# Kernel optimization log

Hardware: AMD Instinct MI355X
Metric: run time of the kernel (lower is better)

## Reference

```python
import jax, jax.numpy as jnp
import numpy as np

D = 256      # d_model
H = 8        # n_heads
L = 6        # n_layers
F = 1024     # ffn_hidden
MAXB = 50    # max_boids
S = MAXB + 3 # seq len: CLS + ctx + predator + boids
B = 4096
VH = 256     # value_hidden_dim
DH = D // H


def setup_inputs() -> dict:
    key = jax.random.key(0)
    ks = jax.random.split(key, 20)
    r = lambda i, shape: jax.random.normal(ks[i], shape, jnp.float32) * 0.02
    return {
        "observation": jax.random.normal(ks[0], (B, 4 + 4 * MAXB), jnp.float32),
        "cls_emb": r(1, (D,)), "type_cls": r(2, (D,)), "type_ctx": r(3, (D,)),
        "type_pred": r(4, (D,)), "type_boid": r(5, (D,)),
        "ctx_W": r(6, (2, D)), "ctx_b": jnp.zeros((D,), jnp.float32),
        "pred_W": r(7, (4, D)), "pred_b": jnp.zeros((D,), jnp.float32),
        "boid_W": r(8, (4, D)), "boid_b": jnp.zeros((D,), jnp.float32),
        "qkv_W": r(9, (L, D, 3 * D)), "qkv_b": jnp.zeros((L, 3 * D), jnp.float32),
        "out_W": r(10, (L, D, D)), "out_b": jnp.zeros((L, D), jnp.float32),
        "ln1_g": jnp.ones((L, D), jnp.float32), "ln1_b": jnp.zeros((L, D), jnp.float32),
        "ffn_W1": r(11, (L, D, F)), "ffn_b1": jnp.zeros((L, F), jnp.float32),
        "ffn_W2": r(12, (L, F, D)), "ffn_b2": jnp.zeros((L, D), jnp.float32),
        "ln2_g": jnp.ones((L, D), jnp.float32), "ln2_b": jnp.zeros((L, D), jnp.float32),
        "proj_W": r(13, (D, 2)), "proj_b": jnp.zeros((2,), jnp.float32),
        "vh_W1": r(14, (D, VH)), "vh_b1": jnp.zeros((VH,), jnp.float32),
        "vh_W2": r(15, (VH, VH)), "vh_b2": jnp.zeros((VH,), jnp.float32),
        "vh_W3": r(16, (VH, 1)), "vh_b3": jnp.zeros((1,), jnp.float32),
    }


def _ln(x, g, b):
    m = jnp.mean(x, axis=-1, keepdims=True)
    v = jnp.mean((x - m) ** 2, axis=-1, keepdims=True)
    return (x - m) * jax.lax.rsqrt(v + 1e-5) * g + b


def reference(observation, cls_emb, type_cls, type_ctx, type_pred, type_boid,
              ctx_W, ctx_b, pred_W, pred_b, boid_W, boid_b,
              qkv_W, qkv_b, out_W, out_b, ln1_g, ln1_b,
              ffn_W1, ffn_b1, ffn_W2, ffn_b2, ln2_g, ln2_b,
              proj_W, proj_b, vh_W1, vh_b1, vh_W2, vh_b2, vh_W3, vh_b3):
    Bn = observation.shape[0]
    ctx = observation[:, :2]                                   # [B,2]
    pred = jnp.concatenate([observation[:, 2:4],
                            jnp.zeros_like(observation[:, :2])], axis=-1)  # [B,4]
    boids = observation[:, 4:].reshape(Bn, MAXB, 4)            # [B,MAXB,4]

    # All-zero boid slots are skipped; valid boids are packed to the front
    # (stable order preserved), then zero-padded -- vectorized via stable argsort.
    valid = jnp.any(boids != 0, axis=-1)                       # [B,MAXB]
    order = jnp.argsort(~valid, axis=1, stable=True)           # valid first
    packed = jnp.take_along_axis(boids, order[:, :, None], axis=1)
    vs = jnp.take_along_axis(valid, order, axis=1)             # [B,MAXB]

    cls_tok = jnp.broadcast_to(cls_emb + type_cls, (Bn, 1, D))
    ctx_tok = (ctx @ ctx_W + ctx_b + type_ctx)[:, None, :]
    pred_tok = (pred @ pred_W + pred_b + type_pred)[:, None, :]
    boid_tok = (packed @ boid_W + boid_b + type_boid) * vs[:, :, None]  # pad -> zeros
    x = jnp.concatenate([cls_tok, ctx_tok, pred_tok, boid_tok], axis=1)  # [B,S,D]

    pad = jnp.concatenate([jnp.zeros((Bn, 3), bool), ~vs], axis=1)       # [B,S]
    neg = jnp.where(pad, -1e9, 0.0)[:, None, None, :]                    # [B,1,1,S]

    scale = 1.0 / np.sqrt(DH)
    for i in range(L):  # post-LN encoder layers (ReLU FFN)
        qkv = x @ qkv_W[i] + qkv_b[i]                                    # [B,S,3D]
        q, k, v = jnp.split(qkv, 3, axis=-1)
        q = q.reshape(Bn, S, H, DH).transpose(0, 2, 1, 3)
        k = k.reshape(Bn, S, H, DH).transpose(0, 2, 1, 3)
        v = v.reshape(Bn, S, H, DH).transpose(0, 2, 1, 3)
        scores = jnp.einsum('bhqd,bhkd->bhqk', q, k) * scale + neg
        a = jax.nn.softmax(scores, axis=-1)
        o = jnp.einsum('bhqk,bhkd->bhqd', a, v).transpose(0, 2, 1, 3).reshape(Bn, S, D)
        x = _ln(x + o @ out_W[i] + out_b[i], ln1_g[i], ln1_b[i])
        h = jax.nn.relu(x @ ffn_W1[i] + ffn_b1[i])
        x = _ln(x + h @ ffn_W2[i] + ffn_b2[i], ln2_g[i], ln2_b[i])

    cls_f = x[:, 0]                                                      # [B,D]
    action_mean = jnp.tanh(cls_f @ proj_W + proj_b)                      # [B,2]
    h = jax.nn.relu(cls_f @ vh_W1 + vh_b1)
    h = jax.nn.relu(h @ vh_W2 + vh_b2)
    value = h @ vh_W3 + vh_b3                                            # [B,1]
    return jnp.concatenate([action_mean, value], axis=-1)                # [B,3]
```

## Files before the change

### kernel.cpp

```cpp
#include <hip/hip_runtime.h>
#include <hip/hip_bf16.h>
#include <stdint.h>

typedef unsigned short u16;
typedef short s16x8 __attribute__((ext_vector_type(8)));
typedef float f32x4 __attribute__((ext_vector_type(4)));

#define D_ 256
#define H_ 8
#define L_ 6
#define F_ 1024
#define MAXB_ 50
#define S_ 53
#define B_ 4096

__device__ __forceinline__ u16 f2b(float f){
  __hip_bfloat16 h = __float2bfloat16(f);
  return *reinterpret_cast<u16*>(&h);
}
__device__ __forceinline__ float b2f(u16 u){
  __hip_bfloat16 h = *reinterpret_cast<__hip_bfloat16*>(&u);
  return __bfloat162float(h);
}

__device__ __forceinline__ void gload16(const void* g, void* l){
  __builtin_amdgcn_global_load_lds((__attribute__((address_space(1))) void*)(g),
                                   (__attribute__((address_space(3))) void*)(l), 16, 0, 0);
}

__global__ __launch_bounds__(256) void prep_weights(
    const float* __restrict__ qkvW, const float* __restrict__ outW,
    const float* __restrict__ w1,   const float* __restrict__ w2,
    u16* __restrict__ qkvT, u16* __restrict__ outT,
    u16* __restrict__ w1T,  u16* __restrict__ w2T)
{
  const int i = blockIdx.x * 256 + threadIdx.x;
  if (i < L_*768*256) {
    const int l = i / (768*256); const int r = i % (768*256);
    const int n = r >> 8; const int k = r & 255;
    qkvT[i] = f2b(qkvW[((size_t)l*256 + k)*768 + n]);
  }
  if (i < L_*256*256) {
    const int l = i >> 16; const int r = i & 65535;
    const int n = r >> 8; const int k = r & 255;
    outT[i] = f2b(outW[((size_t)l*256 + k)*256 + n]);
  }
  if (i < L_*1024*256) {
    const int l = i / (1024*256); const int r = i % (1024*256);
    const int n = r >> 8; const int k = r & 255;
    w1T[i] = f2b(w1[((size_t)l*256 + k)*1024 + n]);
  }
  if (i < L_*256*1024) {
    const int l = i / (256*1024); const int r = i % (256*1024);
    const int n = r >> 10; const int k = r & 1023;
    w2T[i] = f2b(w2[((size_t)l*1024 + k)*256 + n]);
  }
}

__global__ __launch_bounds__(256) void embed_kernel(
    const float* __restrict__ obs,
    const float* __restrict__ cls_emb, const float* __restrict__ type_cls,
    const float* __restrict__ type_ctx, const float* __restrict__ type_pred,
    const float* __restrict__ type_boid,
    const float* __restrict__ ctxW, const float* __restrict__ ctxb,
    const float* __restrict__ predW, const float* __restrict__ predb,
    const float* __restrict__ boidW, const float* __restrict__ boidb,
    u16* __restrict__ xbf, int* __restrict__ nvalid)
{
  const int b = blockIdx.x, tid = threadIdx.x;
  __shared__ float obs_s[204];
  __shared__ int perm_s[MAXB_];
  __shared__ int count_s;
  const float* orow = obs + (size_t)b * 204;
  if (tid < 204) obs_s[tid] = orow[tid];
  __syncthreads();
  if (tid < 64) {
    const int j = tid;
    bool flag = false;
    if (j < MAXB_) {
      const float a0=obs_s[4+4*j], a1=obs_s[5+4*j], a2=obs_s[6+4*j], a3=obs_s[7+4*j];
      flag = (a0!=0.f)||(a1!=0.f)||(a2!=0.f)||(a3!=0.f);
    }
    const unsigned long long m = __ballot(flag);
    if (flag) perm_s[__popcll(m & ((1ull<<j)-1ull))] = j;
    if (j == 0) { count_s = __popcll(m); nvalid[b] = __popcll(m); }
  }
  __syncthreads();
  const int cnt = count_s;
  const int d = tid;
  for (int s = 0; s < S_; ++s) {
    float v;
    if (s == 0)      v = cls_emb[d] + type_cls[d];
    else if (s == 1) v = obs_s[0]*ctxW[d] + obs_s[1]*ctxW[256+d] + ctxb[d] + type_ctx[d];
    else if (s == 2) v = obs_s[2]*predW[d] + obs_s[3]*predW[256+d] + predb[d] + type_pred[d];
    else {
      const int j = s - 3;
      if (j < cnt) {
        const int bj = perm_s[j];
        v = obs_s[4+4*bj]*boidW[d] + obs_s[5+4*bj]*boidW[256+d]
          + obs_s[6+4*bj]*boidW[512+d] + obs_s[7+4*bj]*boidW[768+d]
          + boidb[d] + type_boid[d];
      } else v = 0.f;
    }
    xbf[((size_t)b*S_ + s)*256 + d] = f2b(v);
  }
}

template<bool RELU>
__global__ __launch_bounds__(256, 2) void gemm_bias_kernel(
    const u16* __restrict__ A, const u16* __restrict__ Bt,
    const float* __restrict__ bias, u16* __restrict__ C,
    int N, int K)
{
  __shared__ __attribute__((aligned(16))) u16 As[2][128*64];
  __shared__ __attribute__((aligned(16))) u16 Bs[2][128*64];
  const int tid = threadIdx.x;
  const int w = tid >> 6, lane = tid & 63;
  const int wr = w >> 1, wc = w & 1;
  const int lm = lane & 15, lg = lane >> 4;
  const int lrow = lane >> 3;
  const int lxor = ((lane & 7) ^ lrow) * 8;
  const int m0 = blockIdx.x * 128, n0 = blockIdx.y * 128;
  const int cb0 = (lg*16) ^ ((lm & 7) << 4);
  const int cb1 = (64 + lg*16) ^ ((lm & 7) << 4);

  f32x4 acc[4][4];
  #pragma unroll
  for (int m=0;m<4;m++)
    #pragma unroll
    for (int n=0;n<4;n++)
      #pragma unroll
      for (int t=0;t<4;t++) acc[m][n][t] = 0.f;

  #pragma unroll
  for (int j=0;j<4;j++){
    const int chunk = w*4 + j;
    const int row = chunk*8 + lrow;
    gload16(A  + (size_t)(m0+row)*K + lxor, &As[0][chunk*512]);
    gload16(Bt + (size_t)(n0+row)*K + lxor, &Bs[0][chunk*512]);
  }
  __syncthreads();

  const int NT = K >> 6;
  for (int t = 0; t < NT; ++t) {
    const int cur = t & 1;
    if (t + 1 < NT) {
      const int k0 = (t+1) << 6;
      #pragma unroll
      for (int j=0;j<4;j++){
        const int chunk = w*4 + j;
        const int row = chunk*8 + lrow;
        gload16(A  + (size_t)(m0+row)*K + k0 + lxor, &As[cur^1][chunk*512]);
        gload16(Bt + (size_t)(n0+row)*K + k0 + lxor, &Bs[cur^1][chunk*512]);
      }
    }
    const char* Ab = (const char*)As[cur];
    const char* Bb = (const char*)Bs[cur];
    #pragma unroll
    for (int kk=0;kk<2;kk++){
      const int cb = kk ? cb1 : cb0;
      s16x8 af[4], bfr[4];
      #pragma unroll
      for (int m=0;m<4;m++) af[m]  = *reinterpret_cast<const s16x8*>(Ab + (wr*64 + m*16 + lm)*128 + cb);
      #pragma unroll
      for (int n=0;n<4;n++) bfr[n] = *reinterpret_cast<const s16x8*>(Bb + (wc*64 + n*16 + lm)*128 + cb);
      #pragma unroll
      for (int m=0;m<4;m++)
        #pragma unroll
        for (int n=0;n<4;n++)
          acc[m][n] = __builtin_amdgcn_mfma_f32_16x16x32_bf16(af[m], bfr[n], acc[m][n], 0, 0, 0);
    }
    __syncthreads();
  }

  #pragma unroll
  for (int n=0;n<4;n++){
    const int col = n0 + wc*64 + n*16 + lm;
    const float bv = bias[col];
    #pragma unroll
    for (int m=0;m<4;m++){
      const int r0 = m0 + wr*64 + m*16 + lg*4;
      #pragma unroll
      for (int j=0;j<4;j++){
        float v = acc[m][n][j] + bv;
        if (RELU) v = fmaxf(v, 0.f);
        C[(size_t)(r0+j)*N + col] = f2b(v);
      }
    }
  }
}

__global__ __launch_bounds__(64) void attn_kernel(
    const u16* __restrict__ qkv, u16* __restrict__ O, const int* __restrict__ nvalid)
{
  const int bh = blockIdx.x;
  const int b = bh >> 3, h = bh & 7;
  const int lane = threadIdx.x;
  const int lm = lane & 15, lg = lane >> 4;
  __shared__ __attribute__((aligned(16))) u16 Pl[64*72];
  __shared__ __attribute__((aligned(16))) u16 VT[32*72];
  const size_t base = (size_t)b * S_ * 768;

  s16x8 aQ[4], aK[4];
  #pragma unroll
  for (int t=0;t<4;t++){
    const int r = t*16 + lm;
    if (r < S_){
      aQ[t] = *reinterpret_cast<const s16x8*>(&qkv[base + (size_t)r*768 +       h*32 + lg*8]);
      aK[t] = *reinterpret_cast<const s16x8*>(&qkv[base + (size_t)r*768 + 256 + h*32 + lg*8]);
    } else {
      #pragma unroll
      for (int i=0;i<8;i++){ aQ[t][i]=0; aK[t][i]=0; }
    }
  }
  {
    const int s = lane;
    #pragma unroll
    for (int i4=0;i4<4;i4++){
      s16x8 v;
      if (s < S_) v = *reinterpret_cast<const s16x8*>(&qkv[base + (size_t)s*768 + 512 + h*32 + i4*8]);
      else {
        #pragma unroll
        for (int i=0;i<8;i++) v[i]=0;
      }
      #pragma unroll
      for (int t=0;t<8;t++) VT[(i4*8+t)*72 + s] = (u16)v[t];
    }
  }
  f32x4 zf;
  #pragma unroll
  for (int t=0;t<4;t++) zf[t] = 0.f;
  f32x4 sc[4][4];
  #pragma unroll
  for (int qi=0;qi<4;qi++)
    #pragma unroll
    for (int kj=0;kj<4;kj++)
      sc[qi][kj] = __builtin_amdgcn_mfma_f32_16x16x32_bf16(aQ[qi], aK[kj], zf, 0, 0, 0);

  const int T = 3 + nvalid[b];
  const float scale = 0.17677669529663689f;
  __syncthreads();

  #pragma unroll
  for (int qi=0;qi<4;qi++){
    #pragma unroll
    for (int j=0;j<4;j++){
      float v[4];
      #pragma unroll
      for (int kj=0;kj<4;kj++)
        v[kj] = sc[qi][kj][j]*scale + ((kj*16+lm) < T ? 0.f : -1e9f);
      float mx = fmaxf(fmaxf(v[0],v[1]), fmaxf(v[2],v[3]));
      mx = fmaxf(mx, __shfl_xor(mx, 1));
      mx = fmaxf(mx, __shfl_xor(mx, 2));
      mx = fmaxf(mx, __shfl_xor(mx, 4));
      mx = fmaxf(mx, __shfl_xor(mx, 8));
      float e[4]; float sum = 0.f;
      #pragma unroll
      for (int kj=0;kj<4;kj++){ e[kj] = __expf(v[kj]-mx); sum += e[kj]; }
      sum += __shfl_xor(sum, 1);
      sum += __shfl_xor(sum, 2);
      sum += __shfl_xor(sum, 4);
      sum += __shfl_xor(sum, 8);
      const float inv = 1.f / sum;
      const int q = qi*16 + lg*4 + j;
      #pragma unroll
      for (int kj=0;kj<4;kj++) Pl[q*72 + kj*16 + lm] = f2b(e[kj]*inv);
    }
  }
  __syncthreads();

  s16x8 bV[2][2];
  #pragma unroll
  for (int c=0;c<2;c++)
    #pragma unroll
    for (int dj=0;dj<2;dj++)
      bV[c][dj] = *reinterpret_cast<const s16x8*>(&VT[(dj*16+lm)*72 + c*32 + lg*8]);

  f32x4 oa[4][2];
  #pragma unroll
  for (int qi=0;qi<4;qi++)
    #pragma unroll
    for (int dj=0;dj<2;dj++)
      #pragma unroll
      for (int t=0;t<4;t++) oa[qi][dj][t] = 0.f;

  #pragma unroll
  for (int qi=0;qi<4;qi++){
    #pragma unroll
    for (int c=0;c<2;c++){
      const s16x8 aP = *reinterpret_cast<const s16x8*>(&Pl[(qi*16+lm)*72 + c*32 + lg*8]);
      #pragma unroll
      for (int dj=0;dj<2;dj++)
        oa[qi][dj] = __builtin_amdgcn_mfma_f32_16x16x32_bf16(aP, bV[c][dj], oa[qi][dj], 0, 0, 0);
    }
  }
  #pragma unroll
  for (int qi=0;qi<4;qi++)
    #pragma unroll
    for (int dj=0;dj<2;dj++)
      #pragma unroll
      for (int j=0;j<4;j++){
        const int q = qi*16 + lg*4 + j;
        if (q < S_)
          O[((size_t)(b*S_ + q))*256 + h*32 + dj*16 + lm] = f2b(oa[qi][dj][j]);
      }
}

__global__ __launch_bounds__(512, 2) void gemm_ln_kernel(
    const u16* __restrict__ A, const u16* __restrict__ Bt,
    const float* __restrict__ bias, const float* __restrict__ lng, const float* __restrict__ lnb,
    u16* __restrict__ xbf, int K)
{
  __shared__ __attribute__((aligned(16))) u16 As[2][128*64];
  __shared__ __attribute__((aligned(16))) u16 Bs[2][256*64];
  __shared__ float redS[4][128];
  __shared__ float redQ[4][128];
  const int tid = threadIdx.x;
  const int w = tid >> 6, lane = tid & 63;
  const int wr = w >> 2, wc = w & 3;
  const int lm = lane & 15, lg = lane >> 4;
  const int lrow = lane >> 3;
  const int lxor = ((lane & 7) ^ lrow) * 8;
  const int m0 = blockIdx.x * 128;
  const int cb0 = (lg*16) ^ ((lm & 7) << 4);
  const int cb1 = (64 + lg*16) ^ ((lm & 7) << 4);

  f32x4 acc[4][4];
  #pragma unroll
  for (int m=0;m<4;m++)
    #pragma unroll
    for (int n=0;n<4;n++)
      #pragma unroll
      for (int t=0;t<4;t++) acc[m][n][t] = 0.f;

  #pragma unroll
  for (int j=0;j<2;j++){
    const int chunk = w*2 + j;
    gload16(A + (size_t)(m0 + chunk*8 + lrow)*K + lxor, &As[0][chunk*512]);
  }
  #pragma unroll
  for (int j=0;j<4;j++){
    const int chunk = w*4 + j;
    gload16(Bt + (size_t)(chunk*8 + lrow)*K + lxor, &Bs[0][chunk*512]);
  }
  __syncthreads();

  const int NT = K >> 6;
  for (int t = 0; t < NT; ++t) {
    const int cur = t & 1;
    if (t + 1 < NT) {
      const int k0 = (t+1) << 6;
      #pragma unroll
      for (int j=0;j<2;j++){
        const int chunk = w*2 + j;
        gload16(A + (size_t)(m0 + chunk*8 + lrow)*K + k0 + lxor, &As[cur^1][chunk*512]);
      }
      #pragma unroll
      for (int j=0;j<4;j++){
        const int chunk = w*4 + j;
        gload16(Bt + (size_t)(chunk*8 + lrow)*K + k0 + lxor, &Bs[cur^1][chunk*512]);
      }
    }
    const char* Ab = (const char*)As[cur];
    const char* Bb = (const char*)Bs[cur];
    #pragma unroll
    for (int kk=0;kk<2;kk++){
      const int cb = kk ? cb1 : cb0;
      s16x8 af[4], bfr[4];
      #pragma unroll
      for (int m=0;m<4;m++) af[m]  = *reinterpret_cast<const s16x8*>(Ab + (wr*64 + m*16 + lm)*128 + cb);
      #pragma unroll
      for (int n=0;n<4;n++) bfr[n] = *reinterpret_cast<const s16x8*>(Bb + (wc*64 + n*16 + lm)*128 + cb);
      #pragma unroll
      for (int m=0;m<4;m++)
        #pragma unroll
        for (int n=0;n<4;n++)
          acc[m][n] = __builtin_amdgcn_mfma_f32_16x16x32_bf16(af[m], bfr[n], acc[m][n], 0, 0, 0);
    }
    __syncthreads();
  }

  float bb[4];
  #pragma unroll
  for (int n=0;n<4;n++) bb[n] = bias[wc*64 + n*16 + lm];
  #pragma unroll
  for (int m=0;m<4;m++)
    #pragma unroll
    for (int j=0;j<4;j++){
      const int r = wr*64 + m*16 + lg*4 + j;
      const u16* resp = xbf + (size_t)(m0+r)*256 + wc*64 + lm;
      #pragma unroll
      for (int n=0;n<4;n++) acc[m][n][j] += bb[n] + b2f(resp[n*16]);
    }

  #pragma unroll
  for (int m=0;m<4;m++)
    #pragma unroll
    for (int j=0;j<4;j++){
      float s1 = 0.f, s2 = 0.f;
      #pragma unroll
      for (int n=0;n<4;n++){ const float t2 = acc[m][n][j]; s1 += t2; s2 += t2*t2; }
      s1 += __shfl_xor(s1, 1); s2 += __shfl_xor(s2, 1);
      s1 += __shfl_xor(s1, 2); s2 += __shfl_xor(s2, 2);
      s1 += __shfl_xor(s1, 4); s2 += __shfl_xor(s2, 4);
      s1 += __shfl_xor(s1, 8); s2 += __shfl_xor(s2, 8);
      if (lm == 0){ const int r = wr*64 + m*16 + lg*4 + j; redS[wc][r] = s1; redQ[wc][r] = s2; }
    }
  __syncthreads();

  float gg[4], be[4];
  #pragma unroll
  for (int n=0;n<4;n++){ const int col = wc*64 + n*16 + lm; gg[n] = lng[col]; be[n] = lnb[col]; }
  #pragma unroll
  for (int m=0;m<4;m++)
    #pragma unroll
    for (int j=0;j<4;j++){
      const int r = wr*64 + m*16 + lg*4 + j;
      const float sum = redS[0][r]+redS[1][r]+redS[2][r]+redS[3][r];
      const float sq  = redQ[0][r]+redQ[1][r]+redQ[2][r]+redQ[3][r];
      const float mean = sum * (1.f/256.f);
      const float var  = sq  * (1.f/256.f) - mean*mean;
      const float rstd = rsqrtf(var + 1e-5f);
      #pragma unroll
      for (int n=0;n<4;n++){
        const float y = (acc[m][n][j] - mean)*rstd*gg[n] + be[n];
        xbf[(size_t)(m0+r)*256 + wc*64 + n*16 + lm] = f2b(y);
      }
    }
}

__global__ __launch_bounds__(256) void head_kernel(
    const u16* __restrict__ xbf,
    const float* __restrict__ projW, const float* __restrict__ projb,
    const float* __restrict__ W1, const float* __restrict__ b1,
    const float* __restrict__ W2, const float* __restrict__ b2,
    const float* __restrict__ W3, const float* __restrict__ b3,
    float* __restrict__ out)
{
  const int b = blockIdx.x, tid = threadIdx.x;
  __shared__ float c_s[256];
  __shared__ float h_s[256];
  __shared__ float red[3][4];
  const float c = b2f(xbf[((size_t)b*S_)*256 + tid]);
  c_s[tid] = c;
  __syncthreads();
  float a1 = b1[tid];
  #pragma unroll 8
  for (int k=0;k<256;k++) a1 += c_s[k]*W1[k*256+tid];
  a1 = fmaxf(a1, 0.f);
  h_s[tid] = a1;
  __syncthreads();
  float a2 = b2[tid];
  #pragma unroll 8
  for (int k=0;k<256;k++) a2 += h_s[k]*W2[k*256+tid];
  a2 = fmaxf(a2, 0.f);

  float pv = a2 * W3[tid];
  float p0 = c * projW[tid*2];
  float p1 = c * projW[tid*2+1];
  #pragma unroll
  for (int o=1;o<64;o<<=1){
    pv += __shfl_xor(pv, o);
    p0 += __shfl_xor(p0, o);
    p1 += __shfl_xor(p1, o);
  }
  const int w = tid >> 6;
  if ((tid & 63) == 0){ red[0][w]=p0; red[1][w]=p1; red[2][w]=pv; }
  __syncthreads();
  if (tid == 0){
    const float q0 = red[0][0]+red[0][1]+red[0][2]+red[0][3] + projb[0];
    const float q1 = red[1][0]+red[1][1]+red[1][2]+red[1][3] + projb[1];
    const float qv = red[2][0]+red[2][1]+red[2][2]+red[2][3] + b3[0];
    out[b*3+0] = tanhf(q0);
    out[b*3+1] = tanhf(q1);
    out[b*3+2] = qv;
  }
}

__global__ void fallback_ws(float* out, int n, float val){
  const int i = blockIdx.x*256 + threadIdx.x;
  if (i < n) out[i] = val;
}

extern "C" void kernel_launch(void* const* d_in, const int* in_sizes, int n_in,
                              void* d_out, int out_size, void* d_ws, size_t ws_size,
                              hipStream_t stream)
{
  (void)in_sizes; (void)n_in;
  const float* obs      = (const float*)d_in[0];
  const float* cls_emb  = (const float*)d_in[1];
  const float* type_cls = (const float*)d_in[2];
  const float* type_ctx = (const float*)d_in[3];
  const float* type_pred= (const float*)d_in[4];
  const float* type_boid= (const float*)d_in[5];
  const float* ctx_W    = (const float*)d_in[6];
  const float* ctx_b    = (const float*)d_in[7];
  const float* pred_W   = (const float*)d_in[8];
  const float* pred_b   = (const float*)d_in[9];
  const float* boid_W   = (const float*)d_in[10];
  const float* boid_b   = (const float*)d_in[11];
  const float* qkv_W    = (const float*)d_in[12];
  const float* qkv_b    = (const float*)d_in[13];
  const float* out_W    = (const float*)d_in[14];
  const float* out_b    = (const float*)d_in[15];
  const float* ln1_g    = (const float*)d_in[16];
  const float* ln1_b    = (const float*)d_in[17];
  const float* ffn_W1   = (const float*)d_in[18];
  const float* ffn_b1   = (const float*)d_in[19];
  const float* ffn_W2   = (const float*)d_in[20];
  const float* ffn_b2   = (const float*)d_in[21];
  const float* ln2_g    = (const float*)d_in[22];
  const float* ln2_b    = (const float*)d_in[23];
  const float* proj_W   = (const float*)d_in[24];
  const float* proj_b   = (const float*)d_in[25];
  const float* vh_W1    = (const float*)d_in[26];
  const float* vh_b1    = (const float*)d_in[27];
  const float* vh_W2    = (const float*)d_in[28];
  const float* vh_b2    = (const float*)d_in[29];
  const float* vh_W3    = (const float*)d_in[30];
  const float* vh_b3    = (const float*)d_in[31];

  const size_t SZ_WQ = (size_t)L_*768*256*2;
  const size_t SZ_WO = (size_t)L_*256*256*2;
  const size_t SZ_W1 = (size_t)L_*1024*256*2;
  const size_t SZ_W2 = (size_t)L_*256*1024*2;
  const size_t SZ_W  = SZ_WQ + SZ_WO + SZ_W1 + SZ_W2;

  size_t avail = (ws_size > SZ_W + 8192) ? (ws_size - SZ_W - 8192) : 0;
  long long bcm = (long long)(avail / 135684ull);
  if (bcm > B_) bcm = B_;
  int Bc_max = (int)((bcm / 128) * 128);
  if (Bc_max < 128) {
    const float val = 2000.0f + (float)(ws_size >> 20);
    fallback_ws<<<(out_size+255)/256, 256, 0, stream>>>((float*)d_out, out_size, val);
    return;
  }
  const size_t Mc_max = (size_t)Bc_max * S_;

  char* ws = (char*)d_ws;
  u16* wq  = (u16*)(ws);
  u16* wo  = (u16*)(ws + SZ_WQ);
  u16* w1t = (u16*)(ws + SZ_WQ + SZ_WO);
  u16* w2t = (u16*)(ws + SZ_WQ + SZ_WO + SZ_W1);
  char* act = ws + SZ_W;
  u16* xbf  = (u16*)(act);
  u16* big  = (u16*)(act + Mc_max*512);
  u16* obuf = big + Mc_max*768;
  int* nval = (int*)(act + Mc_max*512 + Mc_max*2048);

  prep_weights<<<6144, 256, 0, stream>>>(qkv_W, out_W, ffn_W1, ffn_W2, wq, wo, w1t, w2t);

  int b0 = 0;
  while (b0 < B_) {
    const int Bc = (B_ - b0 < Bc_max) ? (B_ - b0) : Bc_max;
    const int Mc = Bc * S_;
    embed_kernel<<<Bc, 256, 0, stream>>>(obs + (size_t)b0*204,
        cls_emb, type_cls, type_ctx, type_pred, type_boid,
        ctx_W, ctx_b, pred_W, pred_b, boid_W, boid_b,
        xbf, nval);
    for (int l = 0; l < L_; ++l) {
      gemm_bias_kernel<false><<<dim3(Mc/128, 6), 256, 0, stream>>>(
          xbf, wq + (size_t)l*768*256, qkv_b + l*768, big, 768, 256);
      attn_kernel<<<Bc*H_, 64, 0, stream>>>(big, obuf, nval);
      gemm_ln_kernel<<<Mc/128, 512, 0, stream>>>(
          obuf, wo + (size_t)l*256*256, out_b + l*256, ln1_g + l*256, ln1_b + l*256,
          xbf, 256);
      gemm_bias_kernel<true><<<dim3(Mc/128, 8), 256, 0, stream>>>(
          xbf, w1t + (size_t)l*1024*256, ffn_b1 + l*1024, big, 1024, 256);
      gemm_ln_kernel<<<Mc/128, 512, 0, stream>>>(
          big, w2t + (size_t)l*256*1024, ffn_b2 + l*256, ln2_g + l*256, ln2_b + l*256,
          xbf, 1024);
    }
    head_kernel<<<Bc, 256, 0, stream>>>(xbf, proj_W, proj_b, vh_W1, vh_b1, vh_W2, vh_b2,
                                        vh_W3, vh_b3, (float*)d_out + (size_t)b0*3);
    b0 += Bc;
  }
}
```

Before: 5.532 ms.

## Fuse FFN up/down projections and LayerNorm with hidden activations kept in LDS

Adds an ffn_kernel that computes the ReLU hidden activations for a 64-row tile and stores them in a 128KB swizzled LDS buffer. It then runs the down projection, residual add and LayerNorm in the same launch, so the 1024-wide intermediate never goes to global memory. Both the A tile and the weights are read straight from global/L2 without LDS staging, and the kernel runs one 512-thread block per CU. Separately, gemm_ln_kernel is changed to 64-row tiles with 256 threads and a single LDS buffer, dropping its double-buffered prefetch in exchange for more blocks.

```diff
diff --git a/kernel.cpp b/kernel.cpp
--- a/kernel.cpp
+++ b/kernel.cpp
@@ -306,24 +306,23 @@
       }
 }
 
-__global__ __launch_bounds__(512, 2) void gemm_ln_kernel(
+__global__ __launch_bounds__(256, 2) void gemm_ln_kernel(
     const u16* __restrict__ A, const u16* __restrict__ Bt,
     const float* __restrict__ bias, const float* __restrict__ lng, const float* __restrict__ lnb,
     u16* __restrict__ xbf, int K)
 {
-  __shared__ __attribute__((aligned(16))) u16 As[2][128*64];
-  __shared__ __attribute__((aligned(16))) u16 Bs[2][256*64];
-  __shared__ float redS[4][128];
-  __shared__ float redQ[4][128];
+  __shared__ __attribute__((aligned(16))) u16 As[64*64];
+  __shared__ __attribute__((aligned(16))) u16 Bs[256*64];
+  __shared__ float redS[4][64];
+  __shared__ float redQ[4][64];
   const int tid = threadIdx.x;
   const int w = tid >> 6, lane = tid & 63;
-  const int wr = w >> 2, wc = w & 3;
   const int lm = lane & 15, lg = lane >> 4;
   const int lrow = lane >> 3;
   const int lxor = ((lane & 7) ^ lrow) * 8;
-  const int m0 = blockIdx.x * 128;
-  const int cb0 = (lg*16) ^ ((lm & 7) << 4);
-  const int cb1 = (64 + lg*16) ^ ((lm & 7) << 4);
+  const int m0 = blockIdx.x * 64;
+  const int cb0 = ((lg*16) ^ ((lm & 7) << 4));
+  const int cb1 = ((64 + lg*16) ^ ((lm & 7) << 4));
 
   f32x4 acc[4][4];
   #pragma unroll
@@ -333,44 +332,29 @@
       #pragma unroll
       for (int t=0;t<4;t++) acc[m][n][t] = 0.f;
 
-  #pragma unroll
-  for (int j=0;j<2;j++){
-    const int chunk = w*2 + j;
-    gload16(A + (size_t)(m0 + chunk*8 + lrow)*K + lxor, &As[0][chunk*512]);
-  }
-  #pragma unroll
-  for (int j=0;j<4;j++){
-    const int chunk = w*4 + j;
-    gload16(Bt + (size_t)(chunk*8 + lrow)*K + lxor, &Bs[0][chunk*512]);
-  }
-  __syncthreads();
-
-  const int NT = K >> 6;
-  for (int t = 0; t < NT; ++t) {
-    const int cur = t & 1;
-    if (t + 1 < NT) {
-      const int k0 = (t+1) << 6;
-      #pragma unroll
-      for (int j=0;j<2;j++){
-        const int chunk = w*2 + j;
-        gload16(A + (size_t)(m0 + chunk*8 + lrow)*K + k0 + lxor, &As[cur^1][chunk*512]);
-      }
-      #pragma unroll
-      for (int j=0;j<4;j++){
-        const int chunk = w*4 + j;
-        gload16(Bt + (size_t)(chunk*8 + lrow)*K + k0 + lxor, &Bs[cur^1][chunk*512]);
-      }
-    }
-    const char* Ab = (const char*)As[cur];
-    const char* Bb = (const char*)Bs[cur];
+  const char* Ab = (const char*)As;
+  const char* Bb = (const char*)Bs;
+
+  for (int k0 = 0; k0 < K; k0 += 64) {
+    #pragma unroll
+    for (int j=0;j<2;j++){
+      const int chunk = w*2 + j;
+      gload16(A + (size_t)(m0 + chunk*8 + lrow)*K + k0 + lxor, &As[chunk*512]);
+    }
+    #pragma unroll
+    for (int j=0;j<8;j++){
+      const int chunk = w*8 + j;
+      gload16(Bt + (size_t)(chunk*8 + lrow)*K + k0 + lxor, &Bs[chunk*512]);
+    }
+    __syncthreads();
     #pragma unroll
     for (int kk=0;kk<2;kk++){
       const int cb = kk ? cb1 : cb0;
       s16x8 af[4], bfr[4];
       #pragma unroll
-      for (int m=0;m<4;m++) af[m]  = *reinterpret_cast<const s16x8*>(Ab + (wr*64 + m*16 + lm)*128 + cb);
-      #pragma unroll
-      for (int n=0;n<4;n++) bfr[n] = *reinterpret_cast<const s16x8*>(Bb + (wc*64 + n*16 + lm)*128 + cb);
+      for (int m=0;m<4;m++) af[m]  = *reinterpret_cast<const s16x8*>(Ab + (m*16 + lm)*128 + cb);
+      #pragma unroll
+      for (int n=0;n<4;n++) bfr[n] = *reinterpret_cast<const s16x8*>(Bb + (w*64 + n*16 + lm)*128 + cb);
       #pragma unroll
       for (int m=0;m<4;m++)
         #pragma unroll
@@ -382,13 +366,13 @@
 
   float bb[4];
   #pragma unroll
-  for (int n=0;n<4;n++) bb[n] = bias[wc*64 + n*16 + lm];
+  for (int n=0;n<4;n++) bb[n] = bias[w*64 + n*16 + lm];
   #pragma unroll
   for (int m=0;m<4;m++)
     #pragma unroll
     for (int j=0;j<4;j++){
-      const int r = wr*64 + m*16 + lg*4 + j;
-      const u16* resp = xbf + (size_t)(m0+r)*256 + wc*64 + lm;
+      const int r = m*16 + lg*4 + j;
+      const u16* resp = xbf + (size_t)(m0+r)*256 + w*64 + lm;
       #pragma unroll
       for (int n=0;n<4;n++) acc[m][n][j] += bb[n] + b2f(resp[n*16]);
     }
@@ -404,18 +388,18 @@
       s1 += __shfl_xor(s1, 2); s2 += __shfl_xor(s2, 2);
       s1 += __shfl_xor(s1, 4); s2 += __shfl_xor(s2, 4);
       s1 += __shfl_xor(s1, 8); s2 += __shfl_xor(s2, 8);
-      if (lm == 0){ const int r = wr*64 + m*16 + lg*4 + j; redS[wc][r] = s1; redQ[wc][r] = s2; }
+      if (lm == 0){ const int r = m*16 + lg*4 + j; redS[w][r] = s1; redQ[w][r] = s2; }
     }
   __syncthreads();
 
   float gg[4], be[4];
   #pragma unroll
-  for (int n=0;n<4;n++){ const int col = wc*64 + n*16 + lm; gg[n] = lng[col]; be[n] = lnb[col]; }
+  for (int n=0;n<4;n++){ const int col = w*64 + n*16 + lm; gg[n] = lng[col]; be[n] = lnb[col]; }
   #pragma unroll
   for (int m=0;m<4;m++)
     #pragma unroll
     for (int j=0;j<4;j++){
-      const int r = wr*64 + m*16 + lg*4 + j;
+      const int r = m*16 + lg*4 + j;
       const float sum = redS[0][r]+redS[1][r]+redS[2][r]+redS[3][r];
       const float sq  = redQ[0][r]+redQ[1][r]+redQ[2][r]+redQ[3][r];
       const float mean = sum * (1.f/256.f);
@@ -424,7 +408,137 @@
       #pragma unroll
       for (int n=0;n<4;n++){
         const float y = (acc[m][n][j] - mean)*rstd*gg[n] + be[n];
-        xbf[(size_t)(m0+r)*256 + wc*64 + n*16 + lm] = f2b(y);
+        xbf[(size_t)(m0+r)*256 + w*64 + n*16 + lm] = f2b(y);
+      }
+    }
+}
+
+__global__ __launch_bounds__(512, 1) void ffn_kernel(
+    const u16* __restrict__ xbf_in, u16* __restrict__ xbf,
+    const u16* __restrict__ w1t,  const float* __restrict__ b1,
+    const u16* __restrict__ w2t,  const float* __restrict__ b2,
+    const float* __restrict__ lng, const float* __restrict__ lnb)
+{
+  __shared__ __attribute__((aligned(16))) u16 hls[64*1024];
+  __shared__ float redS[8][64];
+  __shared__ float redQ[8][64];
+  const int tid = threadIdx.x;
+  const int w = tid >> 6, lane = tid & 63;
+  const int lm = lane & 15, lg = lane >> 4;
+  const int m0 = blockIdx.x * 64;
+
+  #pragma unroll
+  for (int ns = 0; ns < 2; ++ns) {
+    const int n0 = w*128 + ns*64;
+    f32x4 acc[4][4];
+    #pragma unroll
+    for (int m=0;m<4;m++)
+      #pragma unroll
+      for (int n=0;n<4;n++)
+        #pragma unroll
+        for (int t=0;t<4;t++) acc[m][n][t] = 0.f;
+    #pragma unroll
+    for (int kf=0; kf<8; ++kf) {
+      s16x8 af[4], bfr[4];
+      #pragma unroll
+      for (int m=0;m<4;m++)
+        af[m] = *reinterpret_cast<const s16x8*>(&xbf_in[(size_t)(m0+m*16+lm)*256 + kf*32 + lg*8]);
+      #pragma unroll
+      for (int n=0;n<4;n++)
+        bfr[n] = *reinterpret_cast<const s16x8*>(&w1t[(size_t)(n0+n*16+lm)*256 + kf*32 + lg*8]);
+      #pragma unroll
+      for (int m=0;m<4;m++)
+        #pragma unroll
+        for (int n=0;n<4;n++)
+          acc[m][n] = __builtin_amdgcn_mfma_f32_16x16x32_bf16(af[m], bfr[n], acc[m][n], 0, 0, 0);
+    }
+    float bb1[4];
+    #pragma unroll
+    for (int n=0;n<4;n++) bb1[n] = b1[n0 + n*16 + lm];
+    #pragma unroll
+    for (int m=0;m<4;m++)
+      #pragma unroll
+      for (int j=0;j<4;j++){
+        const int r = m*16 + lg*4 + j;
+        const int sw = (r & 7) << 3;
+        #pragma unroll
+        for (int n=0;n<4;n++){
+          const int c = n0 + n*16 + lm;
+          hls[r*1024 + (c ^ sw)] = f2b(fmaxf(acc[m][n][j] + bb1[n], 0.f));
+        }
+      }
+  }
+  __syncthreads();
+
+  const int nc0 = w*32;
+  f32x4 a2[4][2];
+  #pragma unroll
+  for (int m=0;m<4;m++)
+    #pragma unroll
+    for (int n=0;n<2;n++)
+      #pragma unroll
+      for (int t=0;t<4;t++) a2[m][n][t] = 0.f;
+  const int swr = (lm & 7) << 3;
+  for (int kf=0; kf<32; ++kf) {
+    s16x8 af[4], bfr[2];
+    #pragma unroll
+    for (int m=0;m<4;m++)
+      af[m] = *reinterpret_cast<const s16x8*>(&hls[(m*16+lm)*1024 + ((kf*32 + lg*8) ^ swr)]);
+    #pragma unroll
+    for (int n=0;n<2;n++)
+      bfr[n] = *reinterpret_cast<const s16x8*>(&w2t[(size_t)(nc0+n*16+lm)*1024 + kf*32 + lg*8]);
+    #pragma unroll
+    for (int m=0;m<4;m++)
+      #pragma unroll
+      for (int n=0;n<2;n++)
+        a2[m][n] = __builtin_amdgcn_mfma_f32_16x16x32_bf16(af[m], bfr[n], a2[m][n], 0, 0, 0);
+  }
+
+  float bb2[2];
+  #pragma unroll
+  for (int n=0;n<2;n++) bb2[n] = b2[nc0 + n*16 + lm];
+  #pragma unroll
+  for (int m=0;m<4;m++)
+    #pragma unroll
+    for (int j=0;j<4;j++){
+      const int r = m*16 + lg*4 + j;
+      const u16* resp = xbf + (size_t)(m0+r)*256 + nc0 + lm;
+      #pragma unroll
+      for (int n=0;n<2;n++) a2[m][n][j] += bb2[n] + b2f(resp[n*16]);
+    }
+  #pragma unroll
+  for (int m=0;m<4;m++)
+    #pragma unroll
+    for (int j=0;j<4;j++){
+      float s1 = 0.f, s2 = 0.f;
+      #pragma unroll
+      for (int n=0;n<2;n++){ const float t2 = a2[m][n][j]; s1 += t2; s2 += t2*t2; }
+      s1 += __shfl_xor(s1, 1); s2 += __shfl_xor(s2, 1);
+      s1 += __shfl_xor(s1, 2); s2 += __shfl_xor(s2, 2);
+      s1 += __shfl_xor(s1, 4); s2 += __shfl_xor(s2, 4);
+      s1 += __shfl_xor(s1, 8); s2 += __shfl_xor(s2, 8);
+      if (lm == 0){ const int r = m*16 + lg*4 + j; redS[w][r] = s1; redQ[w][r] = s2; }
+    }
+  __syncthreads();
+
+  float gg[2], be[2];
+  #pragma unroll
+  for (int n=0;n<2;n++){ const int col = nc0 + n*16 + lm; gg[n] = lng[col]; be[n] = lnb[col]; }
+  #pragma unroll
+  for (int m=0;m<4;m++)
+    #pragma unroll
+    for (int j=0;j<4;j++){
+      const int r = m*16 + lg*4 + j;
+      float sum = 0.f, sq = 0.f;
+      #pragma unroll
+      for (int u=0;u<8;u++){ sum += redS[u][r]; sq += redQ[u][r]; }
+      const float mean = sum * (1.f/256.f);
+      const float var  = sq  * (1.f/256.f) - mean*mean;
+      const float rstd = rsqrtf(var + 1e-5f);
+      #pragma unroll
+      for (int n=0;n<2;n++){
+        const float y = (a2[m][n][j] - mean)*rstd*gg[n] + be[n];
+        xbf[(size_t)(m0+r)*256 + nc0 + n*16 + lm] = f2b(y);
       }
     }
 }
@@ -562,14 +676,14 @@
       gemm_bias_kernel<false><<<dim3(Mc/128, 6), 256, 0, stream>>>(
           xbf, wq + (size_t)l*768*256, qkv_b + l*768, big, 768, 256);
       attn_kernel<<<Bc*H_, 64, 0, stream>>>(big, obuf, nval);
-      gemm_ln_kernel<<<Mc/128, 512, 0, stream>>>(
+      gemm_ln_kernel<<<Mc/64, 256, 0, stream>>>(
           obuf, wo + (size_t)l*256*256, out_b + l*256, ln1_g + l*256, ln1_b + l*256,
           xbf, 256);
-      gemm_bias_kernel<true><<<dim3(Mc/128, 8), 256, 0, stream>>>(
-          xbf, w1t + (size_t)l*1024*256, ffn_b1 + l*1024, big, 1024, 256);
-      gemm_ln_kernel<<<Mc/128, 512, 0, stream>>>(
-          big, w2t + (size_t)l*256*1024, ffn_b2 + l*256, ln2_g + l*256, ln2_b + l*256,
-          xbf, 1024);
+      ffn_kernel<<<Mc/64, 512, 0, stream>>>(
+          xbf, xbf,
+          w1t + (size_t)l*1024*256, ffn_b1 + l*1024,
+          w2t + (size_t)l*256*1024, ffn_b2 + l*256,
+          ln2_g + l*256, ln2_b + l*256);
     }
     head_kernel<<<Bc, 256, 0, stream>>>(xbf, proj_W, proj_b, vh_W1, vh_b1, vh_W2, vh_b2,
                                         vh_W3, vh_b3, (float*)d_out + (size_t)b0*3);
```

Measured after the change: 7.146 ms. 29.2% more time.
